# Kernel optimization log

Measured on AMD Instinct MI355X. Metric: run time of the kernel, lower is better.

The kernel has to match this reference:

```python
import jax, jax.numpy as jnp
import numpy as np

D_MODEL = 256
N_LEVELS = 4
N_HEADS = 8
N_POINTS = 4
LEN_Q = 1024
LEN_X = 256
SHAPES_NP = np.array([[100, 100], [50, 50], [25, 25], [13, 13]], dtype=np.int32)
LEN_IN = int((SHAPES_NP[:, 0] * SHAPES_NP[:, 1]).sum())  # 13294


def setup_inputs() -> dict:
    key = jax.random.key(0)
    ks = jax.random.split(key, 10)
    s = 0.02
    lvl_start = np.concatenate([[0], np.cumsum(SHAPES_NP[:, 0] * SHAPES_NP[:, 1])[:-1]]).astype(np.int32)
    return {
        "query": jax.random.normal(ks[0], (1, LEN_Q, D_MODEL), jnp.float32),
        "reference_points": jax.random.uniform(ks[1], (1, LEN_Q, N_LEVELS, 2), jnp.float32),
        "input_flatten": jax.random.normal(ks[2], (1, LEN_IN, D_MODEL), jnp.float32),
        "input_spatial_shapes": jnp.asarray(SHAPES_NP, jnp.int32),
        "add_keys": jax.random.normal(ks[3], (1, LEN_X, D_MODEL), jnp.float32),
        "input_level_start_index": jnp.asarray(lvl_start, jnp.int32),
        "W_off": jax.random.normal(ks[4], (N_HEADS * N_LEVELS * N_POINTS * 2, D_MODEL), jnp.float32) * s,
        "b_off": jax.random.normal(ks[5], (N_HEADS * N_LEVELS * N_POINTS * 2,), jnp.float32),
        "W_attn": jax.random.normal(ks[6], (N_HEADS * (N_LEVELS + 1), D_MODEL, D_MODEL), jnp.float32) * s,
        "W_val": jax.random.normal(ks[7], (2 * N_HEADS, D_MODEL, D_MODEL), jnp.float32) * s,
        "b_val": jax.random.normal(ks[8], (2 * N_HEADS, D_MODEL), jnp.float32) * s,
        "W_mix": jax.random.normal(ks[9], (D_MODEL, N_HEADS + 1), jnp.float32) * s,
    }


def reference(query, reference_points, input_flatten, input_spatial_shapes, add_keys,
              input_level_start_index, W_off, b_off, W_attn, W_val, b_val, W_mix):
    N, Lq, C = query.shape
    H, L, P = N_HEADS, N_LEVELS, N_POINTS

    # sampling offsets: (N, Lq, H, L, P, 2)
    off = (query @ W_off.T + b_off).reshape(N, Lq, H, L, P, 2)
    iss_f = input_spatial_shapes.astype(jnp.float32)          # (L, 2) = (H_l, W_l)
    wh = iss_f[:, ::-1]                                        # (W_l, H_l)
    loc = reference_points[:, :, None, :, None, :] + off / wh[None, None, None, :, None, :]

    # get_keys: clamp, quantize to int index (matches torch .int() trunc, values >= 0)
    loc = jnp.clip(loc, 0.0, 0.999)
    idx = (loc * iss_f[None, None, None, :, None, :]).astype(jnp.int32)
    h_l = input_spatial_shapes[:, 0]                           # (L,)
    flat_idx = (idx[..., 0] + idx[..., 1] * h_l[None, None, None, :, None]
                + input_level_start_index[None, None, None, :, None])   # (N, Lq, H, L, P)
    keys = input_flatten[0][flat_idx[0]]                       # (Lq, H, L, P, C)
    keys = jnp.transpose(keys, (1, 2, 3, 0, 4))                # (H, L, P, Lq, C)

    q = query.reshape(Lq, C)
    head_w = jax.nn.softmax(W_mix.T, axis=0)                   # (H+1, C), softmax over heads
    result = q * head_w[-1][None]
    addk = add_keys.reshape(-1, C)                             # (Lx, C)

    for h in range(H):
        attn = []
        for lvl in range(L):
            simil = W_attn[h * L + lvl]
            # faithful to torch: (C, P*Lq) row-major reshaped to (P, Lq, C)
            ki = (simil @ keys[h, lvl].reshape(-1, C).T).reshape(P, Lq, C)
            attn.append((ki * q[None]).sum(-1))                # (P, Lq)
        simil = W_attn[h * L + L]
        ki = addk @ simil.T                                    # (Lx, C)
        attn.append(ki @ q.T)                                  # (Lx, Lq)
        attn = jax.nn.softmax(jnp.concatenate(attn, axis=0), axis=0)  # (L*P+Lx, Lq)

        vals = (keys[h].reshape(-1, C) @ W_val[2 * h].T + b_val[2 * h]).reshape(L * P, Lq, C)
        v2 = addk @ W_val[2 * h + 1].T + b_val[2 * h + 1]      # (Lx, C)
        vals = jnp.concatenate([vals, jnp.broadcast_to(v2[:, None], (v2.shape[0], Lq, C))], axis=0)
        result = result + (attn[:, :, None] * vals).sum(0) * head_w[h][None]

    return result[None]
```

## Files before the change

kernel.cpp:

```cpp
#include <hip/hip_runtime.h>

typedef unsigned short ushort_t;
typedef __attribute__((ext_vector_type(8))) short bh8;
typedef __attribute__((ext_vector_type(4))) float f4;
typedef __attribute__((ext_vector_type(4))) unsigned int u4;

__device__ __forceinline__ ushort_t f2bf(float f) {
  unsigned u = __float_as_uint(f);
  return (ushort_t)((u + 0x7FFFu + ((u >> 16) & 1u)) >> 16);
}
__device__ __forceinline__ float bf2f(ushort_t v) {
  return __uint_as_float(((unsigned)v) << 16);
}

template <typename OutT>
__device__ __forceinline__ void gemm_abt_core(
    char* smem,
    const ushort_t* __restrict__ A, const ushort_t* __restrict__ B,
    OutT* __restrict__ C, int ldA, int ldB, int ldC, int K, int m0, int n0)
{
  ushort_t* As = (ushort_t*)smem;
  ushort_t* Bs = (ushort_t*)(smem + 10240);
  int t = threadIdx.x;
  int lane = t & 63, w = t >> 6;
  int quad = lane >> 4, l15 = lane & 15;
  int wm = w >> 1, wn = w & 1;
  f4 acc[4][4];
  #pragma unroll
  for (int mi = 0; mi < 4; ++mi)
    #pragma unroll
    for (int ni = 0; ni < 4; ++ni) acc[mi][ni] = (f4)0.f;
  int row = t >> 1, kh = (t & 1) * 16;
  for (int k0 = 0; k0 < K; k0 += 32) {
    if (k0) __syncthreads();
    {
      const u4* ga = (const u4*)(A + (m0 + row) * ldA + k0 + kh);
      u4 v0 = ga[0], v1 = ga[1];
      u4* da = (u4*)(As + row * 40 + kh); da[0] = v0; da[1] = v1;
      const u4* gb = (const u4*)(B + (n0 + row) * ldB + k0 + kh);
      u4 u0 = gb[0], u1 = gb[1];
      u4* db = (u4*)(Bs + row * 40 + kh); db[0] = u0; db[1] = u1;
    }
    __syncthreads();
    bh8 af[4], bfv[4];
    #pragma unroll
    for (int mi = 0; mi < 4; ++mi)
      af[mi] = *(bh8*)(As + (wm * 64 + mi * 16 + l15) * 40 + quad * 8);
    #pragma unroll
    for (int ni = 0; ni < 4; ++ni)
      bfv[ni] = *(bh8*)(Bs + (wn * 64 + ni * 16 + l15) * 40 + quad * 8);
    #pragma unroll
    for (int mi = 0; mi < 4; ++mi)
      #pragma unroll
      for (int ni = 0; ni < 4; ++ni)
        acc[mi][ni] = __builtin_amdgcn_mfma_f32_16x16x32_bf16(af[mi], bfv[ni], acc[mi][ni], 0, 0, 0);
  }
  #pragma unroll
  for (int mi = 0; mi < 4; ++mi)
    #pragma unroll
    for (int ni = 0; ni < 4; ++ni)
      #pragma unroll
      for (int r = 0; r < 4; ++r) {
        int mg = m0 + wm * 64 + mi * 16 + quad * 4 + r;
        int ng = n0 + wn * 64 + ni * 16 + l15;
        if constexpr (sizeof(OutT) == 4) C[mg * ldC + ng] = acc[mi][ni][r];
        else C[mg * ldC + ng] = (OutT)f2bf(acc[mi][ni][r]);
      }
}

__global__ __launch_bounds__(256) void k_fused_cast_off(
    const float* __restrict__ q, const float* __restrict__ xin,
    const float* __restrict__ addk, const float* __restrict__ Wval,
    const float* __restrict__ Wattn, ushort_t* __restrict__ arena,
    const float* __restrict__ Woff, float* __restrict__ off_buf)
{
  if (blockIdx.x < 2048) {
    const int total4 = 1850240;
    for (int i = blockIdx.x * 256 + threadIdx.x; i < total4; i += 2048 * 256) {
      const float* src; ushort_t* dst; int e;
      if (i < 65536)        { src = q    + i * 4;            dst = arena + i * 4; }
      else if (i < 916352)  { e = i - 65536;  src = xin  + e * 4; dst = arena + 262144  + e * 4; }
      else if (i < 932736)  { e = i - 916352; src = addk + e * 4; dst = arena + 3665408 + e * 4; }
      else if (i < 1194880) {
        e = i - 932736; int el = e * 4;
        int h = el >> 17, r = el & 131071;
        int c = r >> 9, k = r & 511;
        src = Wval + (2 * h + (k >> 8)) * 65536 + c * 256 + (k & 255);
        dst = arena + 3730944 + el;
      }
      else if (i < 1325952) {
        e = i - 1194880; int el = e * 4;
        int h = el >> 16, off = el & 65535;
        src = Wattn + h * 262144 + 262144 + off;
        dst = arena + 5828096 + el;
      }
      else {
        e = i - 1325952;
        src = Wattn + e * 4;
        dst = arena + 6352384 + e * 4;
      }
      float4 v = *(const float4*)src;
      ushort4 o; o.x = f2bf(v.x); o.y = f2bf(v.y); o.z = f2bf(v.z); o.w = f2bf(v.w);
      *(ushort4*)dst = o;
    }
  } else {
    __shared__ float As[16][65];
    __shared__ float Bs[16][65];
    int e = blockIdx.x - 2048;
    int nx = e & 3, my = e >> 2;
    int m0 = my * 64, n0 = nx * 64;
    int t = threadIdx.x;
    int tm = t & 15, tn = t >> 4;
    int lr = t >> 4, lc = t & 15;
    float acc[4][4] = {};
    for (int k0 = 0; k0 < 256; k0 += 16) {
      #pragma unroll
      for (int i = 0; i < 4; ++i) {
        int r = lr + i * 16;
        As[lc][r] = q[(m0 + r) * 256 + k0 + lc];
        Bs[lc][r] = Woff[(n0 + r) * 256 + k0 + lc];
      }
      __syncthreads();
      #pragma unroll
      for (int k = 0; k < 16; ++k) {
        float a[4], b[4];
        #pragma unroll
        for (int i = 0; i < 4; ++i) a[i] = As[k][tm * 4 + i];
        #pragma unroll
        for (int j = 0; j < 4; ++j) b[j] = Bs[k][tn * 4 + j];
        #pragma unroll
        for (int i = 0; i < 4; ++i)
          #pragma unroll
          for (int j = 0; j < 4; ++j) acc[i][j] += a[i] * b[j];
      }
      __syncthreads();
    }
    #pragma unroll
    for (int i = 0; i < 4; ++i)
      #pragma unroll
      for (int j = 0; j < 4; ++j)
        off_buf[(m0 + tm * 4 + i) * 256 + n0 + tn * 4 + j] = acc[i][j];
  }
}

__global__ __launch_bounds__(256) void k_fused_idx_g4(
    const float* __restrict__ off_buf, const float* __restrict__ boff,
    const float* __restrict__ refpts, const int* __restrict__ shapes,
    const int* __restrict__ lvlst, int* __restrict__ fidx,
    const ushort_t* __restrict__ addk, const ushort_t* __restrict__ Wattn4,
    ushort_t* __restrict__ tmp)
{
  __shared__ __align__(16) char smem[20480];
  if (blockIdx.x < 512) {
    int t = threadIdx.x;
    int b = blockIdx.x * 2 + (t >> 7), tt = t & 127;
    int l = (tt >> 2) & 3;
    float off0 = off_buf[b * 256 + 2 * tt]     + boff[2 * tt];
    float off1 = off_buf[b * 256 + 2 * tt + 1] + boff[2 * tt + 1];
    int Hi = shapes[2 * l], Wi = shapes[2 * l + 1];
    float Hf = (float)Hi, Wf = (float)Wi;
    float r0 = refpts[b * 8 + 2 * l], r1 = refpts[b * 8 + 2 * l + 1];
    float l0 = fminf(fmaxf(r0 + off0 / Wf, 0.f), 0.999f);
    float l1 = fminf(fmaxf(r1 + off1 / Hf, 0.f), 0.999f);
    int i0 = (int)(l0 * Hf);
    int i1 = (int)(l1 * Wf);
    fidx[b * 128 + tt] = i0 + i1 * Hi + lvlst[l];
  } else {
    int e = blockIdx.x - 512;
    int h = e >> 2, rem = e & 3, my = rem >> 1, nx = rem & 1;
    gemm_abt_core<ushort_t>(smem, addk, Wattn4 + h * 65536, tmp + h * 65536,
                            256, 256, 256, 256, my * 128, nx * 128);
  }
}

__device__ __forceinline__ void attn_mfma_body(
    char* smemc,
    const ushort_t* __restrict__ qbf, const ushort_t* __restrict__ xbf,
    const ushort_t* __restrict__ Wlvl, const int* __restrict__ fidx,
    float* __restrict__ attnP, int bx)
{
  unsigned* Bs = (unsigned*)smemc;
  ushort_t* As = (ushort_t*)(smemc + 8704);
  int* fis = (int*)(smemc + 17920);
  float* Nlds = (float*)smemc;

  int h = bx >> 8, l = (bx >> 6) & 3, g = bx & 63;
  int ch = g & 3, g2 = g >> 2;
  int p = g2 >> 2, tg = g2 & 3;
  int c0 = ch * 64;
  int t = threadIdx.x;
  int lane = t & 63, w = t >> 6;
  int quad = lane >> 4, l15 = lane & 15;
  int qcol = p * 4 + tg;
  fis[t] = fidx[(tg * 256 + t) * 128 + h * 16 + l * 4 + p];
  __syncthreads();
  f4 acc[4];
  #pragma unroll
  for (int mi = 0; mi < 4; ++mi) acc[mi] = (f4)0.f;

  int cl = t & 63, sg = t >> 6;
  for (int jt = 0; jt < 4; ++jt) {
    if (jt) __syncthreads();
    unsigned vv[16];
    #pragma unroll
    for (int rr = 0; rr < 16; ++rr)
      vv[rr] = xbf[fis[jt * 64 + sg * 16 + rr] * 256 + c0 + cl];
    #pragma unroll
    for (int i = 0; i < 4; ++i) {
      uint2 w2; w2.x = vv[i * 4] | (vv[i * 4 + 1] << 16);
      w2.y = vv[i * 4 + 2] | (vv[i * 4 + 3] << 16);
      *(uint2*)&Bs[cl * 34 + sg * 8 + i * 2] = w2;
    }
    {
      int u = t >> 2, jj0 = (t & 3) * 16;
      const u4* src = (const u4*)(qbf + (u * 16 + qcol) * 256 + jt * 64 + jj0);
      u4 s0 = src[0], s1 = src[1];
      u4* dst = (u4*)(As + u * 72 + jj0);
      dst[0] = s0; dst[1] = s1;
    }
    __syncthreads();
    #pragma unroll
    for (int ks = 0; ks < 2; ++ks) {
      bh8 af[4], bfv;
      #pragma unroll
      for (int mi = 0; mi < 4; ++mi)
        af[mi] = *(bh8*)(As + (mi * 16 + l15) * 72 + ks * 32 + quad * 8);
      {
        const unsigned* bp = &Bs[(w * 16 + l15) * 34 + ks * 16 + quad * 4];
        uint2 b0 = *(const uint2*)bp;
        uint2 b1 = *(const uint2*)(bp + 2);
        u4 bb; bb.x = b0.x; bb.y = b0.y; bb.z = b1.x; bb.w = b1.y;
        bfv = __builtin_bit_cast(bh8, bb);
      }
      #pragma unroll
      for (int mi = 0; mi < 4; ++mi)
        acc[mi] = __builtin_amdgcn_mfma_f32_16x16x32_bf16(af[mi], bfv, acc[mi], 0, 0, 0);
    }
  }
  __syncthreads();
  #pragma unroll
  for (int mi = 0; mi < 4; ++mi)
    *(f4*)&Nlds[(w * 16 + l15) * 68 + mi * 16 + quad * 4] = acc[mi];
  __syncthreads();
  {
    int a = t >> 6, u = t & 63;
    const ushort_t* Wr = Wlvl + (h * 4 + l) * 65536 + (a * 64 + u) * 256 + c0;
    float s = 0.f;
    #pragma unroll
    for (int cc = 0; cc < 8; ++cc) {
      u4 wv = *(const u4*)(Wr + cc * 8);
      int cb = cc * 8;
      s += __uint_as_float(wv.x << 16)         * Nlds[(cb + 0) * 68 + u];
      s += __uint_as_float(wv.x & 0xffff0000u) * Nlds[(cb + 1) * 68 + u];
      s += __uint_as_float(wv.y << 16)         * Nlds[(cb + 2) * 68 + u];
      s += __uint_as_float(wv.y & 0xffff0000u) * Nlds[(cb + 3) * 68 + u];
      s += __uint_as_float(wv.z << 16)         * Nlds[(cb + 4) * 68 + u];
      s += __uint_as_float(wv.z & 0xffff0000u) * Nlds[(cb + 5) * 68 + u];
      s += __uint_as_float(wv.w << 16)         * Nlds[(cb + 6) * 68 + u];
      s += __uint_as_float(wv.w & 0xffff0000u) * Nlds[(cb + 7) * 68 + u];
    }
    attnP[ch * 131072 + (h * 16 + l * 4 + a) * 1024 + u * 16 + qcol] = s;
  }
}

__global__ __launch_bounds__(256) void k_fused_attn(
    const ushort_t* __restrict__ qbf, const ushort_t* __restrict__ xbf,
    const ushort_t* __restrict__ Wlvl, const int* __restrict__ fidx,
    float* __restrict__ attnP,
    const ushort_t* __restrict__ tmp, float* __restrict__ attn)
{
  __shared__ __align__(16) char smem[20480];
  int bx = blockIdx.x;
  if (bx < 2048) {
    attn_mfma_body(smem, qbf, xbf, Wlvl, fidx, attnP, bx);
  } else {
    int e = bx - 2048;
    int h = e >> 4, rem = e & 15, my = rem >> 3, nx = rem & 7;
    gemm_abt_core<float>(smem, tmp + h * 65536, qbf, attn + h * 278528 + 16384,
                         256, 256, 1024, 256, my * 128, nx * 128);
  }
}

__global__ __launch_bounds__(256) void k_softmax(
    float* __restrict__ attn, const float* __restrict__ attnP,
    ushort_t* __restrict__ attn2bf, float* __restrict__ s1, float* __restrict__ s2)
{
  __shared__ float red[8][32];
  int h = blockIdx.y;
  int b = blockIdx.x * 32 + (threadIdx.x & 31);
  int rg = threadIdx.x >> 5;
  const int R0 = rg * 34;
  float* col = attn + h * 278528 + b;
  float v[34];
  float m = -1e30f;
  #pragma unroll
  for (int i = 0; i < 34; ++i) {
    int r = R0 + i;
    float x;
    if (r < 16) {
      int idx = (h * 16 + r) * 1024 + b;
      x = attnP[idx] + attnP[131072 + idx] + attnP[262144 + idx] + attnP[393216 + idx];
    } else {
      x = col[r * 1024];
    }
    v[i] = x;
    m = fmaxf(m, x);
  }
  red[rg][threadIdx.x & 31] = m;
  __syncthreads();
  #pragma unroll
  for (int j = 0; j < 8; ++j) m = fmaxf(m, red[j][threadIdx.x & 31]);
  float sum = 0.f;
  #pragma unroll
  for (int i = 0; i < 34; ++i) { v[i] = expf(v[i] - m); sum += v[i]; }
  __syncthreads();
  red[rg][threadIdx.x & 31] = sum;
  __syncthreads();
  float tot = 0.f;
  #pragma unroll
  for (int j = 0; j < 8; ++j) tot += red[j][threadIdx.x & 31];
  float inv = 1.f / tot;
  #pragma unroll
  for (int i = 0; i < 34; ++i) {
    int r = R0 + i;
    float x = v[i] * inv;
    if (r < 16) col[r * 1024] = x;
    else attn2bf[h * 262144 + (r - 16) * 1024 + b] = f2bf(x);
  }
  if (rg == 0) {
    float sa = 0.f;
    #pragma unroll
    for (int i = 0; i < 16; ++i) sa += v[i];
    float sn = sa * inv;
    s1[h * 1024 + b] = sn;
    s2[h * 1024 + b] = 1.f - sn;
  }
}

__global__ __launch_bounds__(256) void k_fused_kbar_tn(
    const ushort_t* __restrict__ xbf, const float* __restrict__ attn,
    const int* __restrict__ fidx, const ushort_t* __restrict__ attn2,
    const ushort_t* __restrict__ addk, ushort_t* __restrict__ kabar)
{
  __shared__ __align__(16) unsigned Asu[128 * 20];
  __shared__ __align__(16) unsigned Bsu[128 * 20];
  if (blockIdx.x < 1024) {
    int h = blockIdx.x >> 7, b0 = (blockIdx.x & 127) * 8;
    int t = threadIdx.x;
    int qi = t >> 5, oct = t & 31;
    int b = b0 + qi;
    float sacc[8] = {};
    #pragma unroll
    for (int r = 0; r < 16; ++r) {
      float aw = attn[(h * 272 + r) * 1024 + b];
      int row = fidx[b * 128 + h * 16 + r];
      u4 v = *(const u4*)(xbf + row * 256 + oct * 8);
      sacc[0] += aw * __uint_as_float(v.x << 16);
      sacc[1] += aw * __uint_as_float(v.x & 0xffff0000u);
      sacc[2] += aw * __uint_as_float(v.y << 16);
      sacc[3] += aw * __uint_as_float(v.y & 0xffff0000u);
      sacc[4] += aw * __uint_as_float(v.z << 16);
      sacc[5] += aw * __uint_as_float(v.z & 0xffff0000u);
      sacc[6] += aw * __uint_as_float(v.w << 16);
      sacc[7] += aw * __uint_as_float(v.w & 0xffff0000u);
    }
    u4 o;
    o.x = (unsigned)f2bf(sacc[0]) | ((unsigned)f2bf(sacc[1]) << 16);
    o.y = (unsigned)f2bf(sacc[2]) | ((unsigned)f2bf(sacc[3]) << 16);
    o.z = (unsigned)f2bf(sacc[4]) | ((unsigned)f2bf(sacc[5]) << 16);
    o.w = (unsigned)f2bf(sacc[6]) | ((unsigned)f2bf(sacc[7]) << 16);
    *(u4*)(kabar + (h * 1024 + b) * 512 + oct * 8) = o;
  } else {
    int e = blockIdx.x - 1024;
    int h = e >> 4, rem = e & 15, my = rem >> 1, nx = rem & 1;
    const ushort_t* A = attn2 + h * 262144;
    const ushort_t* B = addk;
    ushort_t* C = kabar + h * 524288;
    int m0 = my * 128, n0 = nx * 128;
    int t = threadIdx.x;
    int lane = t & 63, w = t >> 6;
    int quad = lane >> 4, l15 = lane & 15;
    int wm = w >> 1, wn = w & 1;
    f4 acc[4][4];
    #pragma unroll
    for (int mi = 0; mi < 4; ++mi)
      #pragma unroll
      for (int ni = 0; ni < 4; ++ni) acc[mi][ni] = (f4)0.f;
    int col = t & 127, half = t >> 7;
    for (int k0 = 0; k0 < 256; k0 += 32) {
      if (k0) __syncthreads();
      #pragma unroll
      for (int i = 0; i < 4; ++i) {
        int kpp = half * 4 + i;
        int kk = k0 + kpp * 4;
        unsigned x0 = A[(kk + 0) * 1024 + m0 + col];
        unsigned x1 = A[(kk + 1) * 1024 + m0 + col];
        unsigned x2 = A[(kk + 2) * 1024 + m0 + col];
        unsigned x3 = A[(kk + 3) * 1024 + m0 + col];
        uint2 va; va.x = x0 | (x1 << 16); va.y = x2 | (x3 << 16);
        *(uint2*)&Asu[col * 20 + kpp * 2] = va;
        unsigned y0 = B[(kk + 0) * 256 + n0 + col];
        unsigned y1 = B[(kk + 1) * 256 + n0 + col];
        unsigned y2 = B[(kk + 2) * 256 + n0 + col];
        unsigned y3 = B[(kk + 3) * 256 + n0 + col];
        uint2 vb; vb.x = y0 | (y1 << 16); vb.y = y2 | (y3 << 16);
        *(uint2*)&Bsu[col * 20 + kpp * 2] = vb;
      }
      __syncthreads();
      bh8 af[4], bfv[4];
      #pragma unroll
      for (int mi = 0; mi < 4; ++mi)
        af[mi] = *(bh8*)((const ushort_t*)Asu + (wm * 64 + mi * 16 + l15) * 40 + quad * 8);
      #pragma unroll
      for (int ni = 0; ni < 4; ++ni)
        bfv[ni] = *(bh8*)((const ushort_t*)Bsu + (wn * 64 + ni * 16 + l15) * 40 + quad * 8);
      #pragma unroll
      for (int mi = 0; mi < 4; ++mi)
        #pragma unroll
        for (int ni = 0; ni < 4; ++ni)
          acc[mi][ni] = __builtin_amdgcn_mfma_f32_16x16x32_bf16(af[mi], bfv[ni], acc[mi][ni], 0, 0, 0);
    }
    #pragma unroll
    for (int mi = 0; mi < 4; ++mi)
      #pragma unroll
      for (int ni = 0; ni < 4; ++ni)
        #pragma unroll
        for (int r = 0; r < 4; ++r) {
          int mg = m0 + wm * 64 + mi * 16 + quad * 4 + r;
          int ng = n0 + wn * 64 + ni * 16 + l15;
          C[mg * 512 + 256 + ng] = f2bf(acc[mi][ni][r]);
        }
  }
}

__global__ __launch_bounds__(256) void gemm_val_k(
    const ushort_t* __restrict__ kabar, const ushort_t* __restrict__ Wcat,
    float* __restrict__ Y)
{
  __shared__ __align__(16) char smem[20480];
  int h = blockIdx.z;
  gemm_abt_core<float>(smem, kabar + h * 524288, Wcat + h * 131072, Y + h * 262144,
                       512, 512, 256, 512, blockIdx.y * 128, blockIdx.x * 128);
}

__global__ __launch_bounds__(256) void k_combine(
    const float* __restrict__ q, const float* __restrict__ Wmix,
    const float* __restrict__ Y,
    const float* __restrict__ s1, const float* __restrict__ s2,
    const float* __restrict__ bval, float* __restrict__ out)
{
  int b = blockIdx.x, c = threadIdx.x;
  float w[9];
  float m = -1e30f;
  #pragma unroll
  for (int j = 0; j < 9; ++j) { w[j] = Wmix[c * 9 + j]; m = fmaxf(m, w[j]); }
  float tot = 0.f;
  #pragma unroll
  for (int j = 0; j < 9; ++j) { w[j] = expf(w[j] - m); tot += w[j]; }
  float inv = 1.f / tot;
  float res = q[b * 256 + c] * w[8] * inv;
  #pragma unroll
  for (int hh = 0; hh < 8; ++hh) {
    float y = Y[(hh * 1024 + b) * 256 + c]
            + s1[hh * 1024 + b] * bval[(2 * hh) * 256 + c]
            + s2[hh * 1024 + b] * bval[(2 * hh + 1) * 256 + c];
    res += w[hh] * inv * y;
  }
  out[b * 256 + c] = res;
}

extern "C" void kernel_launch(void* const* d_in, const int* in_sizes, int n_in,
                              void* d_out, int out_size, void* d_ws, size_t ws_size,
                              hipStream_t stream) {
  (void)in_sizes; (void)n_in; (void)out_size; (void)ws_size;
  const float* q      = (const float*)d_in[0];
  const float* refpts = (const float*)d_in[1];
  const float* xin    = (const float*)d_in[2];
  const int*   shapes = (const int*)d_in[3];
  const float* addk   = (const float*)d_in[4];
  const int*   lvlst  = (const int*)d_in[5];
  const float* Woff   = (const float*)d_in[6];
  const float* boff   = (const float*)d_in[7];
  const float* Wattn  = (const float*)d_in[8];
  const float* Wval   = (const float*)d_in[9];
  const float* bval   = (const float*)d_in[10];
  const float* Wmix   = (const float*)d_in[11];
  float* out = (float*)d_out;
  float* ws  = (float*)d_ws;

  int*   fidx    = (int*)ws;
  float* off_buf = ws + 131072;
  float* s1      = ws + 393216;
  float* s2      = ws + 401408;
  float* attn    = ws + 409600;
  float* Y       = ws + 409600;
  ushort_t* arena = (ushort_t*)(ws + 2637824);
  ushort_t* q_bf     = arena;
  ushort_t* xin_bf   = arena + 262144;
  ushort_t* addk_bf  = arena + 3665408;
  ushort_t* Wcat_bf  = arena + 3730944;
  ushort_t* Wattn4_bf= arena + 5828096;
  ushort_t* Wlvl_bf  = arena + 6352384;
  ushort_t* tmp_bf   = arena + 8449536;
  ushort_t* attn2_bf = arena + 8973824;
  ushort_t* kabar_bf = arena + 11070976;
  float* attnP = (float*)(arena + 15265280);

  k_fused_cast_off<<<2112, 256, 0, stream>>>(q, xin, addk, Wval, Wattn, arena,
                                             Woff, off_buf);
  k_fused_idx_g4<<<544, 256, 0, stream>>>(off_buf, boff, refpts, shapes, lvlst,
                                          fidx, addk_bf, Wattn4_bf, tmp_bf);
  k_fused_attn<<<2176, 256, 0, stream>>>(q_bf, xin_bf, Wlvl_bf, fidx, attnP,
                                         tmp_bf, attn);
  k_softmax<<<dim3(32, 8), 256, 0, stream>>>(attn, attnP, attn2_bf, s1, s2);
  k_fused_kbar_tn<<<1152, 256, 0, stream>>>(xin_bf, attn, fidx, attn2_bf,
                                            addk_bf, kabar_bf);
  gemm_val_k<<<dim3(2, 8, 8), 256, 0, stream>>>(kabar_bf, Wcat_bf, Y);
  k_combine<<<1024, 256, 0, stream>>>(q, Wmix, Y, s1, s2, bval, out);
}
```

Measured before the change: 204.9 us.

## Split offset GEMM over K and software-pipeline gathers in attention kernel

The offset projection GEMM is split into two K-halves across twice as many blocks, and the partial sums are written to separate buffers and added in the index kernel. This adds parallelism to the tail blocks of the cast kernel. The attention MFMA body now prefetches the next tile's gathered xin values and q rows into registers before the current tile's MFMAs run, overlapping global gather latency with compute at the cost of more registers. The off_buf is moved into the arena to hold both partials.

```diff
diff --git a/kernel.cpp b/kernel.cpp
--- a/kernel.cpp
+++ b/kernel.cpp
@@ -107,13 +107,15 @@
     __shared__ float As[16][65];
     __shared__ float Bs[16][65];
     int e = blockIdx.x - 2048;
+    int kh2 = e >> 6; e &= 63;
     int nx = e & 3, my = e >> 2;
     int m0 = my * 64, n0 = nx * 64;
+    int kbase = kh2 * 128;
     int t = threadIdx.x;
     int tm = t & 15, tn = t >> 4;
     int lr = t >> 4, lc = t & 15;
     float acc[4][4] = {};
-    for (int k0 = 0; k0 < 256; k0 += 16) {
+    for (int k0 = kbase; k0 < kbase + 128; k0 += 16) {
       #pragma unroll
       for (int i = 0; i < 4; ++i) {
         int r = lr + i * 16;
@@ -139,7 +141,7 @@
     for (int i = 0; i < 4; ++i)
       #pragma unroll
       for (int j = 0; j < 4; ++j)
-        off_buf[(m0 + tm * 4 + i) * 256 + n0 + tn * 4 + j] = acc[i][j];
+        off_buf[kh2 * 262144 + (m0 + tm * 4 + i) * 256 + n0 + tn * 4 + j] = acc[i][j];
   }
 }
 
@@ -155,8 +157,8 @@
     int t = threadIdx.x;
     int b = blockIdx.x * 2 + (t >> 7), tt = t & 127;
     int l = (tt >> 2) & 3;
-    float off0 = off_buf[b * 256 + 2 * tt]     + boff[2 * tt];
-    float off1 = off_buf[b * 256 + 2 * tt + 1] + boff[2 * tt + 1];
+    float off0 = off_buf[b * 256 + 2 * tt]     + off_buf[262144 + b * 256 + 2 * tt]     + boff[2 * tt];
+    float off1 = off_buf[b * 256 + 2 * tt + 1] + off_buf[262144 + b * 256 + 2 * tt + 1] + boff[2 * tt + 1];
     int Hi = shapes[2 * l], Wi = shapes[2 * l + 1];
     float Hf = (float)Hi, Wf = (float)Wi;
     float r0 = refpts[b * 8 + 2 * l], r1 = refpts[b * 8 + 2 * l + 1];
@@ -199,24 +201,32 @@
   for (int mi = 0; mi < 4; ++mi) acc[mi] = (f4)0.f;
 
   int cl = t & 63, sg = t >> 6;
+  int uu = t >> 2, jj0 = (t & 3) * 16;
+  const ushort_t* qrow = qbf + (uu * 16 + qcol) * 256 + jj0;
+
+  unsigned vv[16];
+  u4 a0, a1;
+  #pragma unroll
+  for (int rr = 0; rr < 16; ++rr)
+    vv[rr] = xbf[fis[sg * 16 + rr] * 256 + c0 + cl];
+  { const u4* src = (const u4*)qrow; a0 = src[0]; a1 = src[1]; }
+
+  #pragma unroll
   for (int jt = 0; jt < 4; ++jt) {
     if (jt) __syncthreads();
-    unsigned vv[16];
-    #pragma unroll
-    for (int rr = 0; rr < 16; ++rr)
-      vv[rr] = xbf[fis[jt * 64 + sg * 16 + rr] * 256 + c0 + cl];
     #pragma unroll
     for (int i = 0; i < 4; ++i) {
       uint2 w2; w2.x = vv[i * 4] | (vv[i * 4 + 1] << 16);
       w2.y = vv[i * 4 + 2] | (vv[i * 4 + 3] << 16);
       *(uint2*)&Bs[cl * 34 + sg * 8 + i * 2] = w2;
     }
-    {
-      int u = t >> 2, jj0 = (t & 3) * 16;
-      const u4* src = (const u4*)(qbf + (u * 16 + qcol) * 256 + jt * 64 + jj0);
-      u4 s0 = src[0], s1 = src[1];
-      u4* dst = (u4*)(As + u * 72 + jj0);
-      dst[0] = s0; dst[1] = s1;
+    { u4* dst = (u4*)(As + uu * 72 + jj0); dst[0] = a0; dst[1] = a1; }
+    if (jt < 3) {
+      #pragma unroll
+      for (int rr = 0; rr < 16; ++rr)
+        vv[rr] = xbf[fis[(jt + 1) * 64 + sg * 16 + rr] * 256 + c0 + cl];
+      const u4* src = (const u4*)(qrow + (jt + 1) * 64);
+      a0 = src[0]; a1 = src[1];
     }
     __syncthreads();
     #pragma unroll
@@ -489,7 +499,6 @@
   float* ws  = (float*)d_ws;
 
   int*   fidx    = (int*)ws;
-  float* off_buf = ws + 131072;
   float* s1      = ws + 393216;
   float* s2      = ws + 401408;
   float* attn    = ws + 409600;
@@ -505,8 +514,9 @@
   ushort_t* attn2_bf = arena + 8973824;
   ushort_t* kabar_bf = arena + 11070976;
   float* attnP = (float*)(arena + 15265280);
-
-  k_fused_cast_off<<<2112, 256, 0, stream>>>(q, xin, addk, Wval, Wattn, arena,
+  float* off_buf = (float*)(arena + 16313856);
+
+  k_fused_cast_off<<<2176, 256, 0, stream>>>(q, xin, addk, Wval, Wattn, arena,
                                              Woff, off_buf);
   k_fused_idx_g4<<<544, 256, 0, stream>>>(off_buf, boff, refpts, shapes, lvlst,
                                           fidx, addk_bf, Wattn4_bf, tmp_bf);
```

After: 191.3 us. -6.6%, faster.
